# Performance work log

Hardware: AMD Instinct MI355X
Metric: run time of the kernel (lower is better)

Reference implementation:

```python
import jax, jax.numpy as jnp
import numpy as np

NEG_SLOPE = 0.2  # LeakyReLU slope from the source module


def setup_inputs() -> dict:
    key = jax.random.key(0)
    k_x, k_adj, k_w, k_a = jax.random.split(key, 4)
    N, F_in, F_out, H = 4096, 256, 512, 8
    d = F_out // H
    x = jax.random.normal(k_x, (N, F_in), dtype=jnp.float32)
    adj = jax.random.randint(k_adj, (N, N), 0, 2, dtype=jnp.int32)  # unused by forward, faithful to source
    W = jax.random.normal(k_w, (F_out, F_in), dtype=jnp.float32) * 0.05  # nn.Linear weight [out, in], bias=False
    A = jax.random.normal(k_a, (H, d, d), dtype=jnp.float32) * 0.05      # per-head bilinear attention
    return {"x": x, "adj": adj, "W": W, "A": A}


def reference(x, adj, W, A):
    # x: [N, F_in], W: [F_out, F_in], A: [H, d, d] with F_out = H*d. adj is unused (as in source forward).
    N = x.shape[0]
    H, d, _ = A.shape
    h = (x @ W.T).reshape(N, H, d)                        # [N, H, d]
    q = jnp.einsum('nhd,hde->nhe', h, A)                  # attn_for_self: bilinear projection
    e = jnp.einsum('nhe,mhe->nhm', q, h)                  # attn_for_neighs: [N, H, N] raw scores
    e = jnp.where(e >= 0, e, NEG_SLOPE * e)               # LeakyReLU(0.2)
    attn = jax.nn.softmax(e, axis=-1)                     # normalize over neighbor nodes
    out = jnp.einsum('nhm,mhd->nhd', attn, h)             # weighted neighbor aggregation
    return out.reshape(N, H * d)
```

## Files before the change

kernel.cpp:

```cpp
#include <hip/hip_runtime.h>
#include <stdint.h>


typedef short bf16x8 __attribute__((ext_vector_type(8)));
typedef short short4v __attribute__((ext_vector_type(4)));
typedef float f32x4 __attribute__((ext_vector_type(4)));

#define LOG2E 1.4426950408889634f

__device__ __forceinline__ short f2bf(float f) {
  union { float f; unsigned u; } x;
  x.f = f;
  unsigned r = (x.u + 0x7FFFu + ((x.u >> 16) & 1u)) >> 16;
  return (short)r;
}

__device__ __forceinline__ float rexp2(float x) {
#if __has_builtin(__builtin_amdgcn_exp2f)
  return __builtin_amdgcn_exp2f(x);
#else
  float r;
  asm("v_exp_f32 %0, %1" : "=v"(r) : "v"(x));
  return r;
#endif
}

__device__ __forceinline__ unsigned cvtpk(float lo, float hi) {
  unsigned r;
  asm("v_cvt_pk_bf16_f32 %0, %1, %2" : "=v"(r) : "v"(lo), "v"(hi));
  return r;
}

__global__ __launch_bounds__(256) void prep(const float* __restrict__ xf,
                                            const float* __restrict__ W,
                                            const float* __restrict__ A,
                                            short* __restrict__ xb,
                                            short* __restrict__ Wc) {
  const int b = blockIdx.x;
  if (b < 1024) {
    const int i = (b * 256 + threadIdx.x) * 4;
    float4 v = *(const float4*)(xf + i);
    short4v s = {f2bf(v.x), f2bf(v.y), f2bf(v.z), f2bf(v.w)};
    *(short4v*)(xb + i) = s;
  } else {
    const int r = b - 1024;
    const int k = threadIdx.x;
    if (r < 512) {
      Wc[r * 256 + k] = f2bf(W[r * 256 + k]);
    } else {
      const int rr = r - 512;
      const int head = rr >> 6, e = rr & 63;
      float acc = 0.f;
      for (int dd = 0; dd < 64; ++dd) {
        acc += A[(head * 64 + dd) * 64 + e] * W[(head * 64 + dd) * 256 + k];
      }
      Wc[r * 256 + k] = f2bf(acc * LOG2E);
    }
  }
}

__global__ __launch_bounds__(256) void gemm_hqT(const short* __restrict__ x,
                                                const short* __restrict__ Wc,
                                                short* __restrict__ hq,
                                                short* __restrict__ hT) {
  __shared__ short T[64 * 65];
  const int tid = threadIdx.x;
  const int wave = tid >> 6, lane = tid & 63;
  const int quad = lane >> 4, c = lane & 15;
  const int row0 = blockIdx.y * 64 + wave * 16;
  const int col0 = blockIdx.x * 64;

  f32x4 acc[4];
#pragma unroll
  for (int nt = 0; nt < 4; ++nt) acc[nt] = (f32x4){0.f, 0.f, 0.f, 0.f};
#pragma unroll
  for (int ks = 0; ks < 8; ++ks) {
    bf16x8 a = *(const bf16x8*)(x + (row0 + c) * 256 + ks * 32 + quad * 8);
#pragma unroll
    for (int nt = 0; nt < 4; ++nt) {
      bf16x8 b = *(const bf16x8*)(Wc + (col0 + nt * 16 + c) * 256 + ks * 32 + quad * 8);
      acc[nt] = __builtin_amdgcn_mfma_f32_16x16x32_bf16(a, b, acc[nt], 0, 0, 0);
    }
  }
#pragma unroll
  for (int nt = 0; nt < 4; ++nt)
#pragma unroll
    for (int r = 0; r < 4; ++r) {
      const short v = f2bf(acc[nt][r]);
      hq[(row0 + quad * 4 + r) * 1024 + col0 + nt * 16 + c] = v;
      T[(wave * 16 + quad * 4 + r) * 65 + nt * 16 + c] = v;
    }

  if (blockIdx.x < 8) {
    __syncthreads();
    const int fl = tid >> 2, nch = (tid & 3) * 16;
    short vals[16];
#pragma unroll
    for (int i = 0; i < 16; ++i) vals[i] = T[(nch + i) * 65 + fl];
    bf16x8 lo = {vals[0], vals[1], vals[2], vals[3], vals[4], vals[5], vals[6], vals[7]};
    bf16x8 hi = {vals[8], vals[9], vals[10], vals[11], vals[12], vals[13], vals[14], vals[15]};
    short* dst = hT + (col0 + fl) * 4096 + blockIdx.y * 64 + nch;
    *(bf16x8*)dst = lo;
    *(bf16x8*)(dst + 8) = hi;
  }
}

__global__ __launch_bounds__(256, 4) void attn_split(const short* __restrict__ hq,
                                                     const short* __restrict__ hT,
                                                     short* __restrict__ po,
                                                     float* __restrict__ pl) {
  const int tid = threadIdx.x;
  const int wave = tid >> 6, lane = tid & 63;
  const int quad = lane >> 4, c = lane & 15;
  const int head = blockIdx.y;
  const int q0 = blockIdx.x * 128 + wave * 32;

  __shared__ __align__(16) short K_lds[64 * 68];
  __shared__ __align__(16) short Vt_lds[64 * 68];
  __shared__ __align__(16) short P_lds[4 * 32 * 68];
  short* Pw = &P_lds[wave * 32 * 68];

  bf16x8 qf[2][2];
#pragma unroll
  for (int p = 0; p < 2; ++p) {
    const short* qb = hq + (q0 + p * 16 + c) * 1024 + 512 + head * 64 + quad * 8;
    qf[p][0] = *(const bf16x8*)qb;
    qf[p][1] = *(const bf16x8*)(qb + 32);
  }
  const short one = (short)0x3F80;
  const bf16x8 ones = {one, one, one, one, one, one, one, one};

  f32x4 o[2][4], ol[2];
#pragma unroll
  for (int p = 0; p < 2; ++p) {
#pragma unroll
    for (int mt = 0; mt < 4; ++mt) o[p][mt] = (f32x4){0.f, 0.f, 0.f, 0.f};
    ol[p] = (f32x4){0.f, 0.f, 0.f, 0.f};
  }

  const int kt0 = blockIdx.z * 16;

  const int chunk0 = tid, chunk1 = tid + 256;
  const int key0 = chunk0 >> 3, dc0 = chunk0 & 7;
  const int key1 = chunk1 >> 3, dc1 = chunk1 & 7;
  const short* kp0 = hq + (size_t)(kt0 * 64 + key0) * 1024 + head * 64 + dc0 * 8;
  const short* kp1 = hq + (size_t)(kt0 * 64 + key1) * 1024 + head * 64 + dc1 * 8;
  const short* vp0 = hT + (size_t)(head * 64 + key0) * 4096 + kt0 * 64 + dc0 * 8;
  const short* vp1 = hT + (size_t)(head * 64 + key1) * 4096 + kt0 * 64 + dc1 * 8;
  bf16x8 kr0 = *(const bf16x8*)kp0;
  bf16x8 kr1 = *(const bf16x8*)kp1;
  bf16x8 vr0 = *(const bf16x8*)vp0;
  bf16x8 vr1 = *(const bf16x8*)vp1;

  for (int kt = kt0; kt < kt0 + 16; ++kt) {
    __syncthreads();
    *(bf16x8*)&K_lds[key0 * 68 + dc0 * 8] = kr0;
    *(bf16x8*)&K_lds[key1 * 68 + dc1 * 8] = kr1;
    *(bf16x8*)&Vt_lds[key0 * 68 + dc0 * 8] = vr0;
    *(bf16x8*)&Vt_lds[key1 * 68 + dc1 * 8] = vr1;
    const int adv = (kt + 1 < kt0 + 16) ? 1 : 0;
    kp0 += adv * 65536; kp1 += adv * 65536;
    vp0 += adv * 64;    vp1 += adv * 64;
    kr0 = *(const bf16x8*)kp0;
    kr1 = *(const bf16x8*)kp1;
    vr0 = *(const bf16x8*)vp0;
    vr1 = *(const bf16x8*)vp1;
    __syncthreads();

#pragma unroll
    for (int mt = 0; mt < 4; ++mt) {
      bf16x8 a0 = *(const bf16x8*)&K_lds[(mt * 16 + c) * 68 + quad * 8];
      bf16x8 a1 = *(const bf16x8*)&K_lds[(mt * 16 + c) * 68 + 32 + quad * 8];
#pragma unroll
      for (int p = 0; p < 2; ++p) {
        f32x4 s = (f32x4){0.f, 0.f, 0.f, 0.f};
        s = __builtin_amdgcn_mfma_f32_16x16x32_bf16(a0, qf[p][0], s, 0, 0, 0);
        s = __builtin_amdgcn_mfma_f32_16x16x32_bf16(a1, qf[p][1], s, 0, 0, 0);
        const float p0 = rexp2(fmaxf(s[0], 0.2f * s[0]));
        const float p1 = rexp2(fmaxf(s[1], 0.2f * s[1]));
        const float p2 = rexp2(fmaxf(s[2], 0.2f * s[2]));
        const float p3 = rexp2(fmaxf(s[3], 0.2f * s[3]));
        uint2 d = {cvtpk(p0, p1), cvtpk(p2, p3)};
        *(uint2*)&Pw[(p * 16 + c) * 68 + mt * 16 + quad * 4] = d;
      }
    }
    bf16x8 pb[2][2];
#pragma unroll
    for (int p = 0; p < 2; ++p) {
      short4v r0 = *(const short4v*)&Pw[(p * 16 + c) * 68 + quad * 8];
      short4v r1 = *(const short4v*)&Pw[(p * 16 + c) * 68 + quad * 8 + 4];
      short4v r2 = *(const short4v*)&Pw[(p * 16 + c) * 68 + 32 + quad * 8];
      short4v r3 = *(const short4v*)&Pw[(p * 16 + c) * 68 + 32 + quad * 8 + 4];
      pb[p][0] = (bf16x8){r0[0], r0[1], r0[2], r0[3], r1[0], r1[1], r1[2], r1[3]};
      pb[p][1] = (bf16x8){r2[0], r2[1], r2[2], r2[3], r3[0], r3[1], r3[2], r3[3]};
    }
#pragma unroll
    for (int mt = 0; mt < 4; ++mt) {
      bf16x8 va0 = *(const bf16x8*)&Vt_lds[(mt * 16 + c) * 68 + quad * 8];
      bf16x8 va1 = *(const bf16x8*)&Vt_lds[(mt * 16 + c) * 68 + 32 + quad * 8];
#pragma unroll
      for (int p = 0; p < 2; ++p) {
        o[p][mt] = __builtin_amdgcn_mfma_f32_16x16x32_bf16(va0, pb[p][0], o[p][mt], 0, 0, 0);
        o[p][mt] = __builtin_amdgcn_mfma_f32_16x16x32_bf16(va1, pb[p][1], o[p][mt], 0, 0, 0);
      }
    }
#pragma unroll
    for (int p = 0; p < 2; ++p) {
      ol[p] = __builtin_amdgcn_mfma_f32_16x16x32_bf16(ones, pb[p][0], ol[p], 0, 0, 0);
      ol[p] = __builtin_amdgcn_mfma_f32_16x16x32_bf16(ones, pb[p][1], ol[p], 0, 0, 0);
    }
  }

  const int pbi = (blockIdx.x * 8 + blockIdx.y) * 4 + blockIdx.z;
  short* po_b = po + (size_t)pbi * 8192;
#pragma unroll
  for (int p = 0; p < 2; ++p) {
    const int ql = wave * 32 + p * 16 + c;
#pragma unroll
    for (int mt = 0; mt < 4; ++mt) {
      short4v o4 = {f2bf(o[p][mt][0]), f2bf(o[p][mt][1]),
                    f2bf(o[p][mt][2]), f2bf(o[p][mt][3])};
      *(short4v*)&po_b[ql * 64 + mt * 16 + quad * 4] = o4;
    }
    if (quad == 0) pl[pbi * 128 + ql] = ol[p][0];
  }
}

__global__ __launch_bounds__(256) void merge4(const short* __restrict__ po,
                                              const float* __restrict__ pl,
                                              float* __restrict__ out) {
  const int qt = blockIdx.x, head = blockIdx.y, t = threadIdx.x;
  const int q = t >> 2, dg = t & 3;
  const int q128 = (qt & 1) * 64 + q;
  const int pbb = ((qt >> 1) * 8 + head) * 4;
  const float inv = 1.0f / (pl[pbb * 128 + q128] + pl[(pbb + 1) * 128 + q128] +
                            pl[(pbb + 2) * 128 + q128] + pl[(pbb + 3) * 128 + q128]);
  float a[16];
#pragma unroll
  for (int i = 0; i < 16; ++i) a[i] = 0.f;
#pragma unroll
  for (int z = 0; z < 4; ++z) {
    const short* p = po + (size_t)(pbb + z) * 8192 + q128 * 64 + dg * 16;
    bf16x8 lo = *(const bf16x8*)p;
    bf16x8 hi = *(const bf16x8*)(p + 8);
#pragma unroll
    for (int i = 0; i < 8; ++i) {
      union { unsigned u; float f; } x, y;
      x.u = ((unsigned)(unsigned short)lo[i]) << 16;
      y.u = ((unsigned)(unsigned short)hi[i]) << 16;
      a[i] += x.f;
      a[i + 8] += y.f;
    }
  }
  float* op = out + (qt * 64 + q) * 512 + head * 64 + dg * 16;
#pragma unroll
  for (int i = 0; i < 4; ++i) {
    float4 r = {a[i * 4] * inv, a[i * 4 + 1] * inv, a[i * 4 + 2] * inv, a[i * 4 + 3] * inv};
    *(float4*)(op + i * 4) = r;
  }
}

extern "C" void kernel_launch(void* const* d_in, const int* in_sizes, int n_in,
                              void* d_out, int out_size, void* d_ws, size_t ws_size,
                              hipStream_t stream) {
  const float* x = (const float*)d_in[0];
  const float* W = (const float*)d_in[2];
  const float* A = (const float*)d_in[3];
  for (int i = 0; i < n_in; ++i) {
    if (in_sizes[i] == 4096 * 256) x = (const float*)d_in[i];
    else if (in_sizes[i] == 512 * 256) W = (const float*)d_in[i];
    else if (in_sizes[i] == 8 * 64 * 64) A = (const float*)d_in[i];
  }

  float* out = (float*)d_out;
  short* xb = (short*)d_ws;
  short* Wc = xb + 4096 * 256;
  short* hq = Wc + 1024 * 256;
  short* hT = hq + 4096 * 1024;
  short* po = hT + 512 * 4096;
  float* pl = (float*)(po + (size_t)1024 * 8192);

  prep<<<dim3(2048), dim3(256), 0, stream>>>(x, W, A, xb, Wc);
  gemm_hqT<<<dim3(16, 64), dim3(256), 0, stream>>>(xb, Wc, hq, hT);
  attn_split<<<dim3(32, 8, 4), dim3(256), 0, stream>>>(hq, hT, po, pl);
  merge4<<<dim3(64, 8), dim3(256), 0, stream>>>(po, pl, out);
}
```

Baseline: 178.2 us.

## Permute K rows in LDS so MFMA score output feeds PV directly from registers

```diff
diff --git a/kernel.cpp b/kernel.cpp
--- a/kernel.cpp
+++ b/kernel.cpp
@@ -5,6 +5,7 @@
 typedef short bf16x8 __attribute__((ext_vector_type(8)));
 typedef short short4v __attribute__((ext_vector_type(4)));
 typedef float f32x4 __attribute__((ext_vector_type(4)));
+typedef unsigned u32x4 __attribute__((ext_vector_type(4)));
 
 #define LOG2E 1.4426950408889634f
 
@@ -117,8 +118,6 @@
 
   __shared__ __align__(16) short K_lds[64 * 68];
   __shared__ __align__(16) short Vt_lds[64 * 68];
-  __shared__ __align__(16) short P_lds[4 * 32 * 68];
-  short* Pw = &P_lds[wave * 32 * 68];
 
   bf16x8 qf[2][2];
 #pragma unroll
@@ -140,9 +139,11 @@
 
   const int kt0 = blockIdx.z * 16;
 
-  const int chunk0 = tid, chunk1 = tid + 256;
-  const int key0 = chunk0 >> 3, dc0 = chunk0 & 7;
-  const int key1 = chunk1 >> 3, dc1 = chunk1 & 7;
+  const int key0 = tid >> 3, dc0 = tid & 7;
+  const int key1 = key0 + 32, dc1 = dc0;
+  const int kperm0 = (((key0 >> 2) & 1) << 4) | (((key0 >> 4) & 1) << 3) |
+                     (((key0 >> 3) & 1) << 2) | (key0 & 3);
+  const int kperm1 = kperm0 + 32;
   const short* kp0 = hq + (size_t)(kt0 * 64 + key0) * 1024 + head * 64 + dc0 * 8;
   const short* kp1 = hq + (size_t)(kt0 * 64 + key1) * 1024 + head * 64 + dc1 * 8;
   const short* vp0 = hT + (size_t)(head * 64 + key0) * 4096 + kt0 * 64 + dc0 * 8;
@@ -154,8 +155,8 @@
 
   for (int kt = kt0; kt < kt0 + 16; ++kt) {
     __syncthreads();
-    *(bf16x8*)&K_lds[key0 * 68 + dc0 * 8] = kr0;
-    *(bf16x8*)&K_lds[key1 * 68 + dc1 * 8] = kr1;
+    *(bf16x8*)&K_lds[kperm0 * 68 + dc0 * 8] = kr0;
+    *(bf16x8*)&K_lds[kperm1 * 68 + dc1 * 8] = kr1;
     *(bf16x8*)&Vt_lds[key0 * 68 + dc0 * 8] = vr0;
     *(bf16x8*)&Vt_lds[key1 * 68 + dc1 * 8] = vr1;
     const int adv = (kt + 1 < kt0 + 16) ? 1 : 0;
@@ -167,6 +168,7 @@
     vr1 = *(const bf16x8*)vp1;
     __syncthreads();
 
+    unsigned pw[2][8];
 #pragma unroll
     for (int mt = 0; mt < 4; ++mt) {
       bf16x8 a0 = *(const bf16x8*)&K_lds[(mt * 16 + c) * 68 + quad * 8];
@@ -180,19 +182,17 @@
         const float p1 = rexp2(fmaxf(s[1], 0.2f * s[1]));
         const float p2 = rexp2(fmaxf(s[2], 0.2f * s[2]));
         const float p3 = rexp2(fmaxf(s[3], 0.2f * s[3]));
-        uint2 d = {cvtpk(p0, p1), cvtpk(p2, p3)};
-        *(uint2*)&Pw[(p * 16 + c) * 68 + mt * 16 + quad * 4] = d;
+        pw[p][mt * 2] = cvtpk(p0, p1);
+        pw[p][mt * 2 + 1] = cvtpk(p2, p3);
       }
     }
     bf16x8 pb[2][2];
 #pragma unroll
     for (int p = 0; p < 2; ++p) {
-      short4v r0 = *(const short4v*)&Pw[(p * 16 + c) * 68 + quad * 8];
-      short4v r1 = *(const short4v*)&Pw[(p * 16 + c) * 68 + quad * 8 + 4];
-      short4v r2 = *(const short4v*)&Pw[(p * 16 + c) * 68 + 32 + quad * 8];
-      short4v r3 = *(const short4v*)&Pw[(p * 16 + c) * 68 + 32 + quad * 8 + 4];
-      pb[p][0] = (bf16x8){r0[0], r0[1], r0[2], r0[3], r1[0], r1[1], r1[2], r1[3]};
-      pb[p][1] = (bf16x8){r2[0], r2[1], r2[2], r2[3], r3[0], r3[1], r3[2], r3[3]};
+      u32x4 lo4 = {pw[p][0], pw[p][1], pw[p][2], pw[p][3]};
+      u32x4 hi4 = {pw[p][4], pw[p][5], pw[p][6], pw[p][7]};
+      pb[p][0] = __builtin_bit_cast(bf16x8, lo4);
+      pb[p][1] = __builtin_bit_cast(bf16x8, hi4);
     }
 #pragma unroll
     for (int mt = 0; mt < 4; ++mt) {
```

New measurement: 173.9 us, median of 2. 2.4% less time.
